# Kernel tuning notes

Measured on AMD Instinct MI355X. Metric: run time of the kernel, lower is better.

## Reference

```python
import jax, jax.numpy as jnp
import numpy as np

N_NODES = 100000
N_EDGES = 3200000
IN_FEATS = 512
EDGE_FEATS = 24
OUT_FEATS = 512
LN_EPS = 1e-5


def setup_inputs() -> dict:
    key = jax.random.key(0)
    ks = jax.random.split(key, 8)
    h = jax.random.normal(ks[0], (N_NODES, IN_FEATS), dtype=jnp.float32)
    m = jax.random.normal(ks[1], (N_EDGES, EDGE_FEATS), dtype=jnp.float32)
    dst = jax.random.randint(ks[2], (N_EDGES,), 0, N_NODES, dtype=jnp.int32)
    norm = jax.random.uniform(ks[3], (N_NODES, 1), dtype=jnp.float32)
    stdv = 1.0 / np.sqrt(IN_FEATS + EDGE_FEATS)
    W = jax.random.uniform(ks[4], (OUT_FEATS, IN_FEATS + EDGE_FEATS), dtype=jnp.float32, minval=-stdv, maxval=stdv)
    b = jax.random.uniform(ks[5], (OUT_FEATS,), dtype=jnp.float32, minval=-stdv, maxval=stdv)
    gamma = jnp.ones((OUT_FEATS,), dtype=jnp.float32)
    beta = jnp.zeros((OUT_FEATS,), dtype=jnp.float32)
    return {"h": h, "m": m, "dst": dst, "norm": norm, "W": W, "b": b, "gamma": gamma, "beta": beta}


def reference(h, m, dst, norm, W, b, gamma, beta):
    # copy_e + sum: segment-sum edge features into destination nodes -> [N, 24]
    ah = jax.ops.segment_sum(m, dst, num_segments=N_NODES)
    # scale by per-node norm, concat with node features -> [N, in+24]
    x = jnp.concatenate([h, ah * norm], axis=1)
    # linear
    y = jnp.einsum('nd,od->no', x, W) + b
    # layernorm (elementwise affine)
    mu = jnp.mean(y, axis=-1, keepdims=True)
    var = jnp.mean((y - mu) ** 2, axis=-1, keepdims=True)
    y = gamma * (y - mu) * jax.lax.rsqrt(var + LN_EPS) + beta
    # activation = relu
    return jax.nn.relu(y)
```

## Files before the change

kernel.cpp:

```cpp
#include <hip/hip_runtime.h>
#include <hip/hip_bf16.h>
#include <stdint.h>

#define NN 100000
#define NE 3200000
#define EF 24
#define KF 536
#define BM 64

typedef __attribute__((ext_vector_type(8))) short bf16x8;
typedef __attribute__((ext_vector_type(8))) unsigned short u16x8;
typedef __attribute__((ext_vector_type(4))) float f32x4;

__device__ __forceinline__ unsigned short f2bf(float f) {
  union { float f; unsigned int u; } v; v.f = f;
  unsigned int r = v.u + 0x7FFFu + ((v.u >> 16) & 1u);
  return (unsigned short)(r >> 16);
}

__device__ __forceinline__ void gload_lds16(const void* g, void* l) {
  __builtin_amdgcn_global_load_lds(
      (const __attribute__((address_space(1))) unsigned int*)g,
      (__attribute__((address_space(3))) unsigned int*)l, 16, 0, 0);
}

__global__ void wconv_kernel(const float* __restrict__ W, unsigned short* __restrict__ Wb) {
  int i = blockIdx.x * blockDim.x + threadIdx.x;
  if (i >= 17 * 32 * 64 * 8) return;
  int j = i & 7;
  int lane = (i >> 3) & 63;
  int nt = (i >> 9) & 31;
  int kt = i >> 14;
  int row = nt * 16 + (lane & 15);
  int k = kt * 32 + (lane >> 4) * 8 + j;
  float v = (k < KF) ? W[row * KF + k] : 0.0f;
  Wb[i] = f2bf(v);
}

__global__ __launch_bounds__(256) void init_u64_kernel(unsigned long long* __restrict__ acc) {
  int i = blockIdx.x * 256 + threadIdx.x;
  if (i < NN * 6) acc[i] = 0x4000400040004000ULL;
}

__global__ __launch_bounds__(256) void scatter_u64_kernel(
    const float* __restrict__ m, const int* __restrict__ dst,
    unsigned long long* __restrict__ acc) {
  int i = blockIdx.x * 256 + threadIdx.x;
  if (i >= NE * 6) return;
  int e = i / 6;
  int fp = i - e * 6;
  float4 v = *(const float4*)(m + (size_t)e * EF + fp * 4);
  long long a0 = (long long)__float2int_rn(v.x * 128.f);
  long long a1 = (long long)__float2int_rn(v.y * 128.f);
  long long a2 = (long long)__float2int_rn(v.z * 128.f);
  long long a3 = (long long)__float2int_rn(v.w * 128.f);
  unsigned long long add = (unsigned long long)(a0 + (a1 << 16) + (a2 << 32) + (a3 << 48));
  atomicAdd(acc + (size_t)dst[e] * 6 + fp, add);
}

__global__ __launch_bounds__(256) void decode_u64_kernel(
    const unsigned long long* __restrict__ acc, const float* __restrict__ norm,
    float* __restrict__ ah) {
  int i = blockIdx.x * 256 + threadIdx.x;
  if (i >= NN * 6) return;
  int n = i / 6;
  unsigned long long x = acc[i];
  float nv = norm[n] * (1.0f / 128.0f);
  float4 o;
  o.x = (float)((int)((x >> 0) & 0xFFFF) - 16384) * nv;
  o.y = (float)((int)((x >> 16) & 0xFFFF) - 16384) * nv;
  o.z = (float)((int)((x >> 32) & 0xFFFF) - 16384) * nv;
  o.w = (float)((int)((x >> 48) & 0xFFFF) - 16384) * nv;
  *(float4*)(ah + (size_t)i * 4) = o;
}

__global__ __launch_bounds__(512, 4) void gemm_ln_kernel(
    const float* __restrict__ h, const float* __restrict__ ah,
    const unsigned short* __restrict__ Wb,
    const float* __restrict__ bias, const float* __restrict__ gamma,
    const float* __restrict__ beta, float* __restrict__ out) {
  __shared__ __align__(16) unsigned short Alds[2 * 2048];
  __shared__ __align__(16) unsigned short Blds[2 * 16384];
  __shared__ float red[4][BM][2];
  __shared__ float stats[BM][2];

  const int t = threadIdx.x;
  const int lane = t & 63;
  const int w = t >> 6;
  const int lgrp = lane >> 4;
  const int llow = lane & 15;
  const int mg = w >> 2;
  const int ng = w & 3;
  const int blockRow = blockIdx.x * BM;

  const int am = t >> 3;
  const int c = t & 7;
  const int kkw = c >> 2;
  const int akg = c & 3;
  const int arow = blockRow + am;
  char* aldsdst = (char*)Alds + kkw * 4096 + (((am >> 4) * 64 + akg * 16 + (am & 15)) * 16);

  f32x4 acc[2][8];
#pragma unroll
  for (int i = 0; i < 2; ++i)
#pragma unroll
    for (int j = 0; j < 8; ++j) acc[i][j] = (f32x4){0.f, 0.f, 0.f, 0.f};

  float4 ra0 = make_float4(0.f, 0.f, 0.f, 0.f), ra1 = ra0;
  if (arow < NN) {
    const float* p = h + (size_t)arow * 512 + c * 8;
    ra0 = *(const float4*)p;
    ra1 = *(const float4*)(p + 4);
  }

  for (int step = 0; step < 8; ++step) {
#pragma unroll
    for (int kk = 0; kk < 2; ++kk) {
      const unsigned short* src = Wb + ((size_t)((step * 2 + kk) * 32 + w) * 64 + lane) * 8;
#pragma unroll
      for (int j = 0; j < 4; ++j)
        gload_lds16(src + (size_t)j * 8 * 64 * 8, (char*)Blds + kk * 32768 + (j * 8 + w) * 1024);
    }
    {
      u16x8 bv;
      bv[0] = f2bf(ra0.x); bv[1] = f2bf(ra0.y); bv[2] = f2bf(ra0.z); bv[3] = f2bf(ra0.w);
      bv[4] = f2bf(ra1.x); bv[5] = f2bf(ra1.y); bv[6] = f2bf(ra1.z); bv[7] = f2bf(ra1.w);
      *(u16x8*)aldsdst = bv;
    }
    ra0 = make_float4(0.f, 0.f, 0.f, 0.f); ra1 = ra0;
    if (arow < NN) {
      if (step < 7) {
        const float* p = h + (size_t)arow * 512 + (step + 1) * 64 + c * 8;
        ra0 = *(const float4*)p;
        ra1 = *(const float4*)(p + 4);
      } else if (c < 3) {
        const float* p = ah + (size_t)arow * EF + c * 8;
        ra0 = *(const float4*)p;
        ra1 = *(const float4*)(p + 4);
      }
    }
    __syncthreads();

#pragma unroll
    for (int kk = 0; kk < 2; ++kk) {
      bf16x8 af0 = *(const bf16x8*)((const char*)Alds + kk * 4096 + (((mg * 2 + 0) * 64) + lane) * 16);
      bf16x8 af1 = *(const bf16x8*)((const char*)Alds + kk * 4096 + (((mg * 2 + 1) * 64) + lane) * 16);
#pragma unroll
      for (int j = 0; j < 8; ++j) {
        int nt = ng * 8 + j;
        bf16x8 bf = *(const bf16x8*)((const char*)Blds + kk * 32768 + ((nt * 64) + lane) * 16);
        acc[0][j] = __builtin_amdgcn_mfma_f32_16x16x32_bf16(af0, bf, acc[0][j], 0, 0, 0);
        acc[1][j] = __builtin_amdgcn_mfma_f32_16x16x32_bf16(af1, bf, acc[1][j], 0, 0, 0);
      }
    }
    __syncthreads();
  }

  {
    const unsigned short* src = Wb + ((size_t)(16 * 32 + w) * 64 + lane) * 8;
#pragma unroll
    for (int j = 0; j < 4; ++j)
      gload_lds16(src + (size_t)j * 8 * 64 * 8, (char*)Blds + (j * 8 + w) * 1024);
    if (c < 4) {
      u16x8 bv;
      bv[0] = f2bf(ra0.x); bv[1] = f2bf(ra0.y); bv[2] = f2bf(ra0.z); bv[3] = f2bf(ra0.w);
      bv[4] = f2bf(ra1.x); bv[5] = f2bf(ra1.y); bv[6] = f2bf(ra1.z); bv[7] = f2bf(ra1.w);
      *(u16x8*)((char*)Alds + (((am >> 4) * 64 + akg * 16 + (am & 15)) * 16)) = bv;
    }
    __syncthreads();
    bf16x8 af0 = *(const bf16x8*)((const char*)Alds + (((mg * 2 + 0) * 64) + lane) * 16);
    bf16x8 af1 = *(const bf16x8*)((const char*)Alds + (((mg * 2 + 1) * 64) + lane) * 16);
#pragma unroll
    for (int j = 0; j < 8; ++j) {
      int nt = ng * 8 + j;
      bf16x8 bf = *(const bf16x8*)((const char*)Blds + ((nt * 64) + lane) * 16);
      acc[0][j] = __builtin_amdgcn_mfma_f32_16x16x32_bf16(af0, bf, acc[0][j], 0, 0, 0);
      acc[1][j] = __builtin_amdgcn_mfma_f32_16x16x32_bf16(af1, bf, acc[1][j], 0, 0, 0);
    }
  }

  float bcol[8], gcol[8], btcol[8];
#pragma unroll
  for (int j = 0; j < 8; ++j) {
    int col = (ng * 8 + j) * 16 + llow;
    bcol[j] = bias[col];
    gcol[j] = gamma[col];
    btcol[j] = beta[col];
  }
  float s[2][4], ss[2][4];
#pragma unroll
  for (int mt = 0; mt < 2; ++mt)
#pragma unroll
    for (int r = 0; r < 4; ++r) { s[mt][r] = 0.f; ss[mt][r] = 0.f; }
#pragma unroll
  for (int mt = 0; mt < 2; ++mt)
#pragma unroll
    for (int j = 0; j < 8; ++j)
#pragma unroll
      for (int r = 0; r < 4; ++r) {
        float v = acc[mt][j][r] + bcol[j];
        acc[mt][j][r] = v;
        s[mt][r] += v;
        ss[mt][r] += v * v;
      }
#pragma unroll
  for (int off = 1; off < 16; off <<= 1) {
#pragma unroll
    for (int mt = 0; mt < 2; ++mt)
#pragma unroll
      for (int r = 0; r < 4; ++r) {
        s[mt][r] += __shfl_xor(s[mt][r], off, 64);
        ss[mt][r] += __shfl_xor(ss[mt][r], off, 64);
      }
  }
  if (llow == 0) {
#pragma unroll
    for (int mt = 0; mt < 2; ++mt)
#pragma unroll
      for (int r = 0; r < 4; ++r) {
        int lrow = (mg * 2 + mt) * 16 + lgrp * 4 + r;
        red[ng][lrow][0] = s[mt][r];
        red[ng][lrow][1] = ss[mt][r];
      }
  }
  __syncthreads();
  if (t < BM) {
    float sum = red[0][t][0] + red[1][t][0] + red[2][t][0] + red[3][t][0];
    float sq = red[0][t][1] + red[1][t][1] + red[2][t][1] + red[3][t][1];
    float mean = sum * (1.0f / 512.0f);
    float var = sq * (1.0f / 512.0f) - mean * mean;
    stats[t][0] = mean;
    stats[t][1] = rsqrtf(var + 1e-5f);
  }
  __syncthreads();
#pragma unroll
  for (int mt = 0; mt < 2; ++mt) {
#pragma unroll
    for (int r = 0; r < 4; ++r) {
      int lrow = (mg * 2 + mt) * 16 + lgrp * 4 + r;
      int grow = blockRow + lrow;
      if (grow < NN) {
        float mean = stats[lrow][0];
        float rstd = stats[lrow][1];
#pragma unroll
        for (int j = 0; j < 8; ++j) {
          int col = (ng * 8 + j) * 16 + llow;
          float v = (acc[mt][j][r] - mean) * rstd * gcol[j] + btcol[j];
          out[grow * 512 + col] = fmaxf(v, 0.0f);
        }
      }
    }
  }
}

extern "C" void kernel_launch(void* const* d_in, const int* in_sizes, int n_in,
                              void* d_out, int out_size, void* d_ws, size_t ws_size,
                              hipStream_t stream) {
  const float* h = (const float*)d_in[0];
  const float* m = (const float*)d_in[1];
  const int* dst = (const int*)d_in[2];
  const float* norm = (const float*)d_in[3];
  const float* W = (const float*)d_in[4];
  const float* b = (const float*)d_in[5];
  const float* gamma = (const float*)d_in[6];
  const float* beta = (const float*)d_in[7];
  float* out = (float*)d_out;

  float* ah = (float*)d_ws;
  unsigned short* Wb = (unsigned short*)((char*)d_ws + 9600000);

  unsigned long long* acc = (unsigned long long*)d_out;

  init_u64_kernel<<<(NN * 6 + 255) / 256, 256, 0, stream>>>(acc);
  wconv_kernel<<<(17 * 32 * 64 * 8 + 255) / 256, 256, 0, stream>>>(W, Wb);
  scatter_u64_kernel<<<(NE * 6 + 255) / 256, 256, 0, stream>>>(m, dst, acc);
  decode_u64_kernel<<<(NN * 6 + 255) / 256, 256, 0, stream>>>(acc, norm, ah);
  gemm_ln_kernel<<<(NN + BM - 1) / BM, 512, 0, stream>>>(h, ah, Wb, b, gamma, beta, out);
}
```

Baseline: 361.0 us.

## Overlap edge scatter with node-feature GEMM in one interleaved launch

Splits the computation so the 512-wide h part of the GEMM runs in the same launch as the atomic edge scatter, with GEMM blocks interleaved one in every 25 blocks. Partial fp32 results go to the output buffer, and a second kernel decodes the scattered edge sums straight into LDS, runs the last K-slice, adds the partial results, and applies bias, layernorm and ReLU. The goal is to hide the atomic-bound scatter under GEMM work and drop the separate decode pass and its intermediate buffer. In exchange, the full fp32 output is written and then read back once more, and the two kinds of work compete for the same GPU resources.

```diff
diff --git a/kernel.cpp b/kernel.cpp
--- a/kernel.cpp
+++ b/kernel.cpp
@@ -7,6 +7,10 @@
 #define EF 24
 #define KF 536
 #define BM 64
+#define GSTRIDE 25
+#define NGEMM 1563
+#define NSCAT 37500
+#define NBLK (NGEMM + NSCAT)
 
 typedef __attribute__((ext_vector_type(8))) short bf16x8;
 typedef __attribute__((ext_vector_type(8))) unsigned short u16x8;
@@ -42,45 +46,121 @@
   if (i < NN * 6) acc[i] = 0x4000400040004000ULL;
 }
 
-__global__ __launch_bounds__(256) void scatter_u64_kernel(
-    const float* __restrict__ m, const int* __restrict__ dst,
-    unsigned long long* __restrict__ acc) {
-  int i = blockIdx.x * 256 + threadIdx.x;
-  if (i >= NE * 6) return;
-  int e = i / 6;
-  int fp = i - e * 6;
-  float4 v = *(const float4*)(m + (size_t)e * EF + fp * 4);
-  long long a0 = (long long)__float2int_rn(v.x * 128.f);
-  long long a1 = (long long)__float2int_rn(v.y * 128.f);
-  long long a2 = (long long)__float2int_rn(v.z * 128.f);
-  long long a3 = (long long)__float2int_rn(v.w * 128.f);
-  unsigned long long add = (unsigned long long)(a0 + (a1 << 16) + (a2 << 32) + (a3 << 48));
-  atomicAdd(acc + (size_t)dst[e] * 6 + fp, add);
-}
-
-__global__ __launch_bounds__(256) void decode_u64_kernel(
+__global__ __launch_bounds__(512, 4) void fusedA_kernel(
+    const float* __restrict__ h, const float* __restrict__ m,
+    const int* __restrict__ dst, const unsigned short* __restrict__ Wb,
+    unsigned long long* __restrict__ acc, float* __restrict__ out) {
+  __shared__ __align__(16) unsigned short Alds[2 * 2048];
+  __shared__ __align__(16) unsigned short Blds[2 * 16384];
+
+  const int bid = blockIdx.x;
+  const int t = threadIdx.x;
+
+  if (bid % GSTRIDE != 0) {
+    int sidx = bid - bid / GSTRIDE - 1;
+    int i = sidx * 512 + t;
+    int e = i / 6;
+    int fp = i - e * 6;
+    float4 v = *(const float4*)(m + (size_t)e * EF + fp * 4);
+    long long a0 = (long long)__float2int_rn(v.x * 128.f);
+    long long a1 = (long long)__float2int_rn(v.y * 128.f);
+    long long a2 = (long long)__float2int_rn(v.z * 128.f);
+    long long a3 = (long long)__float2int_rn(v.w * 128.f);
+    unsigned long long add = (unsigned long long)(a0 + (a1 << 16) + (a2 << 32) + (a3 << 48));
+    atomicAdd(acc + (size_t)dst[e] * 6 + fp, add);
+    return;
+  }
+
+  const int g = bid / GSTRIDE;
+  const int lane = t & 63;
+  const int w = t >> 6;
+  const int lgrp = lane >> 4;
+  const int llow = lane & 15;
+  const int mg = w >> 2;
+  const int ng = w & 3;
+  const int blockRow = g * BM;
+
+  const int am = t >> 3;
+  const int c = t & 7;
+  const int kkw = c >> 2;
+  const int akg = c & 3;
+  const int arow = blockRow + am;
+  char* aldsdst = (char*)Alds + kkw * 4096 + (((am >> 4) * 64 + akg * 16 + (am & 15)) * 16);
+
+  f32x4 acc2[2][8];
+#pragma unroll
+  for (int i = 0; i < 2; ++i)
+#pragma unroll
+    for (int j = 0; j < 8; ++j) acc2[i][j] = (f32x4){0.f, 0.f, 0.f, 0.f};
+
+  float4 ra0 = make_float4(0.f, 0.f, 0.f, 0.f), ra1 = ra0;
+  if (arow < NN) {
+    const float* p = h + (size_t)arow * 512 + c * 8;
+    ra0 = *(const float4*)p;
+    ra1 = *(const float4*)(p + 4);
+  }
+
+  for (int step = 0; step < 8; ++step) {
+#pragma unroll
+    for (int kk = 0; kk < 2; ++kk) {
+      const unsigned short* src = Wb + ((size_t)((step * 2 + kk) * 32 + w) * 64 + lane) * 8;
+#pragma unroll
+      for (int j = 0; j < 4; ++j)
+        gload_lds16(src + (size_t)j * 8 * 64 * 8, (char*)Blds + kk * 32768 + (j * 8 + w) * 1024);
+    }
+    {
+      u16x8 bv;
+      bv[0] = f2bf(ra0.x); bv[1] = f2bf(ra0.y); bv[2] = f2bf(ra0.z); bv[3] = f2bf(ra0.w);
+      bv[4] = f2bf(ra1.x); bv[5] = f2bf(ra1.y); bv[6] = f2bf(ra1.z); bv[7] = f2bf(ra1.w);
+      *(u16x8*)aldsdst = bv;
+    }
+    ra0 = make_float4(0.f, 0.f, 0.f, 0.f); ra1 = ra0;
+    if (step < 7 && arow < NN) {
+      const float* p = h + (size_t)arow * 512 + (step + 1) * 64 + c * 8;
+      ra0 = *(const float4*)p;
+      ra1 = *(const float4*)(p + 4);
+    }
+    __syncthreads();
+
+#pragma unroll
+    for (int kk = 0; kk < 2; ++kk) {
+      bf16x8 af0 = *(const bf16x8*)((const char*)Alds + kk * 4096 + (((mg * 2 + 0) * 64) + lane) * 16);
+      bf16x8 af1 = *(const bf16x8*)((const char*)Alds + kk * 4096 + (((mg * 2 + 1) * 64) + lane) * 16);
+#pragma unroll
+      for (int j = 0; j < 8; ++j) {
+        int nt = ng * 8 + j;
+        bf16x8 bf = *(const bf16x8*)((const char*)Blds + kk * 32768 + ((nt * 64) + lane) * 16);
+        acc2[0][j] = __builtin_amdgcn_mfma_f32_16x16x32_bf16(af0, bf, acc2[0][j], 0, 0, 0);
+        acc2[1][j] = __builtin_amdgcn_mfma_f32_16x16x32_bf16(af1, bf, acc2[1][j], 0, 0, 0);
+      }
+    }
+    __syncthreads();
+  }
+
+#pragma unroll
+  for (int mt = 0; mt < 2; ++mt) {
+#pragma unroll
+    for (int r = 0; r < 4; ++r) {
+      int lrow = (mg * 2 + mt) * 16 + lgrp * 4 + r;
+      int grow = blockRow + lrow;
+      if (grow < NN) {
+#pragma unroll
+        for (int j = 0; j < 8; ++j) {
+          int col = (ng * 8 + j) * 16 + llow;
+          out[(size_t)grow * 512 + col] = acc2[mt][j][r];
+        }
+      }
+    }
+  }
+}
+
+__global__ __launch_bounds__(512, 4) void epilogue_kernel(
     const unsigned long long* __restrict__ acc, const float* __restrict__ norm,
-    float* __restrict__ ah) {
-  int i = blockIdx.x * 256 + threadIdx.x;
-  if (i >= NN * 6) return;
-  int n = i / 6;
-  unsigned long long x = acc[i];
-  float nv = norm[n] * (1.0f / 128.0f);
-  float4 o;
-  o.x = (float)((int)((x >> 0) & 0xFFFF) - 16384) * nv;
-  o.y = (float)((int)((x >> 16) & 0xFFFF) - 16384) * nv;
-  o.z = (float)((int)((x >> 32) & 0xFFFF) - 16384) * nv;
-  o.w = (float)((int)((x >> 48) & 0xFFFF) - 16384) * nv;
-  *(float4*)(ah + (size_t)i * 4) = o;
-}
-
-__global__ __launch_bounds__(512, 4) void gemm_ln_kernel(
-    const float* __restrict__ h, const float* __restrict__ ah,
     const unsigned short* __restrict__ Wb,
     const float* __restrict__ bias, const float* __restrict__ gamma,
     const float* __restrict__ beta, float* __restrict__ out) {
-  __shared__ __align__(16) unsigned short Alds[2 * 2048];
-  __shared__ __align__(16) unsigned short Blds[2 * 16384];
+  __shared__ __align__(16) unsigned short Alds[2048];
+  __shared__ __align__(16) unsigned short Blds[16384];
   __shared__ float red[4][BM][2];
   __shared__ float stats[BM][2];
 
@@ -91,91 +171,72 @@
   const int llow = lane & 15;
   const int mg = w >> 2;
   const int ng = w & 3;
-  const int blockRow = blockIdx.x * BM;
-
-  const int am = t >> 3;
-  const int c = t & 7;
-  const int kkw = c >> 2;
-  const int akg = c & 3;
-  const int arow = blockRow + am;
-  char* aldsdst = (char*)Alds + kkw * 4096 + (((am >> 4) * 64 + akg * 16 + (am & 15)) * 16);
-
-  f32x4 acc[2][8];
-#pragma unroll
-  for (int i = 0; i < 2; ++i)
-#pragma unroll
-    for (int j = 0; j < 8; ++j) acc[i][j] = (f32x4){0.f, 0.f, 0.f, 0.f};
-
-  float4 ra0 = make_float4(0.f, 0.f, 0.f, 0.f), ra1 = ra0;
-  if (arow < NN) {
-    const float* p = h + (size_t)arow * 512 + c * 8;
-    ra0 = *(const float4*)p;
-    ra1 = *(const float4*)(p + 4);
-  }
-
-  for (int step = 0; step < 8; ++step) {
-#pragma unroll
-    for (int kk = 0; kk < 2; ++kk) {
-      const unsigned short* src = Wb + ((size_t)((step * 2 + kk) * 32 + w) * 64 + lane) * 8;
-#pragma unroll
-      for (int j = 0; j < 4; ++j)
-        gload_lds16(src + (size_t)j * 8 * 64 * 8, (char*)Blds + kk * 32768 + (j * 8 + w) * 1024);
-    }
-    {
-      u16x8 bv;
-      bv[0] = f2bf(ra0.x); bv[1] = f2bf(ra0.y); bv[2] = f2bf(ra0.z); bv[3] = f2bf(ra0.w);
-      bv[4] = f2bf(ra1.x); bv[5] = f2bf(ra1.y); bv[6] = f2bf(ra1.z); bv[7] = f2bf(ra1.w);
-      *(u16x8*)aldsdst = bv;
-    }
-    ra0 = make_float4(0.f, 0.f, 0.f, 0.f); ra1 = ra0;
-    if (arow < NN) {
-      if (step < 7) {
-        const float* p = h + (size_t)arow * 512 + (step + 1) * 64 + c * 8;
-        ra0 = *(const float4*)p;
-        ra1 = *(const float4*)(p + 4);
-      } else if (c < 3) {
-        const float* p = ah + (size_t)arow * EF + c * 8;
-        ra0 = *(const float4*)p;
-        ra1 = *(const float4*)(p + 4);
-      }
-    }
-    __syncthreads();
-
-#pragma unroll
-    for (int kk = 0; kk < 2; ++kk) {
-      bf16x8 af0 = *(const bf16x8*)((const char*)Alds + kk * 4096 + (((mg * 2 + 0) * 64) + lane) * 16);
-      bf16x8 af1 = *(const bf16x8*)((const char*)Alds + kk * 4096 + (((mg * 2 + 1) * 64) + lane) * 16);
-#pragma unroll
-      for (int j = 0; j < 8; ++j) {
-        int nt = ng * 8 + j;
-        bf16x8 bf = *(const bf16x8*)((const char*)Blds + kk * 32768 + ((nt * 64) + lane) * 16);
-        acc[0][j] = __builtin_amdgcn_mfma_f32_16x16x32_bf16(af0, bf, acc[0][j], 0, 0, 0);
-        acc[1][j] = __builtin_amdgcn_mfma_f32_16x16x32_bf16(af1, bf, acc[1][j], 0, 0, 0);
-      }
-    }
-    __syncthreads();
-  }
+  const int g = blockIdx.x;
+  const int blockRow = g * BM;
 
   {
     const unsigned short* src = Wb + ((size_t)(16 * 32 + w) * 64 + lane) * 8;
 #pragma unroll
     for (int j = 0; j < 4; ++j)
       gload_lds16(src + (size_t)j * 8 * 64 * 8, (char*)Blds + (j * 8 + w) * 1024);
-    if (c < 4) {
-      u16x8 bv;
-      bv[0] = f2bf(ra0.x); bv[1] = f2bf(ra0.y); bv[2] = f2bf(ra0.z); bv[3] = f2bf(ra0.w);
-      bv[4] = f2bf(ra1.x); bv[5] = f2bf(ra1.y); bv[6] = f2bf(ra1.z); bv[7] = f2bf(ra1.w);
-      *(u16x8*)((char*)Alds + (((am >> 4) * 64 + akg * 16 + (am & 15)) * 16)) = bv;
-    }
-    __syncthreads();
+  }
+  if (t < 384) {
+    int row = t / 6;
+    int fp = t - row * 6;
+    int nrow = blockRow + row;
+    unsigned long long x = 0x4000400040004000ULL;
+    float nv = 0.f;
+    if (nrow < NN) {
+      x = acc[(size_t)nrow * 6 + fp];
+      nv = norm[nrow] * (1.0f / 128.0f);
+    }
+    ushort4 o;
+    o.x = f2bf((float)((int)((x >> 0) & 0xFFFF) - 16384) * nv);
+    o.y = f2bf((float)((int)((x >> 16) & 0xFFFF) - 16384) * nv);
+    o.z = f2bf((float)((int)((x >> 32) & 0xFFFF) - 16384) * nv);
+    o.w = f2bf((float)((int)((x >> 48) & 0xFFFF) - 16384) * nv);
+    int akg = fp >> 1;
+    int half = fp & 1;
+    *(ushort4*)((char*)Alds + (((row >> 4) * 64 + akg * 16 + (row & 15)) * 16 + half * 8)) = o;
+  } else {
+    int tt = t - 384;
+    int row = tt >> 1;
+    int half = tt & 1;
+    *(ushort4*)((char*)Alds + (((row >> 4) * 64 + 3 * 16 + (row & 15)) * 16 + half * 8)) =
+        make_ushort4(0, 0, 0, 0);
+  }
+  __syncthreads();
+
+  f32x4 acc2[2][8];
+#pragma unroll
+  for (int i = 0; i < 2; ++i)
+#pragma unroll
+    for (int j = 0; j < 8; ++j) acc2[i][j] = (f32x4){0.f, 0.f, 0.f, 0.f};
+  {
     bf16x8 af0 = *(const bf16x8*)((const char*)Alds + (((mg * 2 + 0) * 64) + lane) * 16);
     bf16x8 af1 = *(const bf16x8*)((const char*)Alds + (((mg * 2 + 1) * 64) + lane) * 16);
 #pragma unroll
     for (int j = 0; j < 8; ++j) {
       int nt = ng * 8 + j;
       bf16x8 bf = *(const bf16x8*)((const char*)Blds + ((nt * 64) + lane) * 16);
-      acc[0][j] = __builtin_amdgcn_mfma_f32_16x16x32_bf16(af0, bf, acc[0][j], 0, 0, 0);
-      acc[1][j] = __builtin_amdgcn_mfma_f32_16x16x32_bf16(af1, bf, acc[1][j], 0, 0, 0);
+      acc2[0][j] = __builtin_amdgcn_mfma_f32_16x16x32_bf16(af0, bf, acc2[0][j], 0, 0, 0);
+      acc2[1][j] = __builtin_amdgcn_mfma_f32_16x16x32_bf16(af1, bf, acc2[1][j], 0, 0, 0);
+    }
+  }
+
+#pragma unroll
+  for (int mt = 0; mt < 2; ++mt) {
+#pragma unroll
+    for (int r = 0; r < 4; ++r) {
+      int lrow = (mg * 2 + mt) * 16 + lgrp * 4 + r;
+      int grow = blockRow + lrow;
+      if (grow < NN) {
+#pragma unroll
+        for (int j = 0; j < 8; ++j) {
+          int col = (ng * 8 + j) * 16 + llow;
+          acc2[mt][j][r] += out[(size_t)grow * 512 + col];
+        }
+      }
     }
   }
 
@@ -198,8 +259,8 @@
     for (int j = 0; j < 8; ++j)
 #pragma unroll
       for (int r = 0; r < 4; ++r) {
-        float v = acc[mt][j][r] + bcol[j];
-        acc[mt][j][r] = v;
+        float v = acc2[mt][j][r] + bcol[j];
+        acc2[mt][j][r] = v;
         s[mt][r] += v;
         ss[mt][r] += v * v;
       }
@@ -245,8 +306,8 @@
 #pragma unroll
         for (int j = 0; j < 8; ++j) {
           int col = (ng * 8 + j) * 16 + llow;
-          float v = (acc[mt][j][r] - mean) * rstd * gcol[j] + btcol[j];
-          out[grow * 512 + col] = fmaxf(v, 0.0f);
+          float v = (acc2[mt][j][r] - mean) * rstd * gcol[j] + btcol[j];
+          out[(size_t)grow * 512 + col] = fmaxf(v, 0.0f);
         }
       }
     }
@@ -266,14 +327,11 @@
   const float* beta = (const float*)d_in[7];
   float* out = (float*)d_out;
 
-  float* ah = (float*)d_ws;
-  unsigned short* Wb = (unsigned short*)((char*)d_ws + 9600000);
-
-  unsigned long long* acc = (unsigned long long*)d_out;
+  unsigned short* Wb = (unsigned short*)d_ws;
+  unsigned long long* acc = (unsigned long long*)((char*)d_ws + 1048576);
 
   init_u64_kernel<<<(NN * 6 + 255) / 256, 256, 0, stream>>>(acc);
   wconv_kernel<<<(17 * 32 * 64 * 8 + 255) / 256, 256, 0, stream>>>(W, Wb);
-  scatter_u64_kernel<<<(NE * 6 + 255) / 256, 256, 0, stream>>>(m, dst, acc);
-  decode_u64_kernel<<<(NN * 6 + 255) / 256, 256, 0, stream>>>(acc, norm, ah);
-  gemm_ln_kernel<<<(NN + BM - 1) / BM, 512, 0, stream>>>(h, ah, Wb, b, gamma, beta, out);
-}
+  fusedA_kernel<<<NBLK, 512, 0, stream>>>(h, m, dst, Wb, acc, out);
+  epilogue_kernel<<<NGEMM, 512, 0, stream>>>(acc, norm, Wb, b, gamma, beta, out);
+}
```

After: 387.8 us. 1.07x slower.
